# Optimization experiments

Measured on AMD Instinct MI355X. Metric: run time of the kernel, lower is better.

## Reference

```python
import jax, jax.numpy as jnp
import numpy as np

B, N, H, E = 64, 512, 32, 4
N_STEPS = 5
ANNO = 1


def setup_inputs() -> dict:
    key = jax.random.key(0)
    ks = jax.random.split(key, 20)
    sc_h = 1.0 / np.sqrt(H)
    sc_3h = 1.0 / np.sqrt(3 * H)
    sc_ha = 1.0 / np.sqrt(H + ANNO)
    inp = {
        "x": jax.random.normal(ks[0], (B, N, H), jnp.float32),
        "a": jax.random.uniform(ks[1], (B, N, ANNO), jnp.float32),
        "m": jax.random.uniform(ks[2], (B, N, 2 * N * E), jnp.float32),
        # fc_in / fc_out: hidden -> hidden*n_edge (torch Linear: W [out,in])
        "W_in": jax.random.normal(ks[3], (H * E, H), jnp.float32) * sc_h,
        "b_in": jax.random.normal(ks[4], (H * E,), jnp.float32) * sc_h,
        "W_out": jax.random.normal(ks[5], (H * E, H), jnp.float32) * sc_h,
        "b_out": jax.random.normal(ks[6], (H * E,), jnp.float32) * sc_h,
        # GRU-style gates: 3*hidden -> hidden
        "Wz": jax.random.normal(ks[7], (H, 3 * H), jnp.float32) * sc_3h,
        "bz": jax.random.normal(ks[8], (H,), jnp.float32) * sc_3h,
        "Wr": jax.random.normal(ks[9], (H, 3 * H), jnp.float32) * sc_3h,
        "br": jax.random.normal(ks[10], (H,), jnp.float32) * sc_3h,
        "Wt": jax.random.normal(ks[11], (H, 3 * H), jnp.float32) * sc_3h,
        "bt": jax.random.normal(ks[12], (H,), jnp.float32) * sc_3h,
        # output head (task_id not in {18,19}): fc1, fc2
        "W1": jax.random.normal(ks[13], (H, H + ANNO), jnp.float32) * sc_ha,
        "b1": jax.random.normal(ks[14], (H,), jnp.float32) * sc_ha,
        "W2": jax.random.normal(ks[15], (1, H), jnp.float32) * sc_h,
        "b2": jax.random.normal(ks[16], (1,), jnp.float32) * sc_h,
    }
    return inp


def _reorder(s):
    # [B, N, H*E] -> view(B,N,H,E) -> transpose(2,3) -> transpose(1,2) -> [B, E*N, H]
    return s.reshape(B, N, H, E).transpose(0, 3, 1, 2).reshape(B, E * N, H)


def reference(x, a, m, W_in, b_in, W_out, b_out, Wz, bz, Wr, br, Wt, bt, W1, b1, W2, b2):
    m_in = m[:, :, : N * E]   # [B, N, N*E]
    m_out = m[:, :, N * E :]  # [B, N, N*E]
    h = x
    for _ in range(N_STEPS):
        s_in = _reorder(h @ W_in.T + b_in)    # [B, E*N, H]
        s_out = _reorder(h @ W_out.T + b_out)  # [B, E*N, H]
        a_in = jnp.einsum("bnm,bmh->bnh", m_in, s_in)
        a_out = jnp.einsum("bnm,bmh->bnh", m_out, s_out)
        cat = jnp.concatenate([a_in, a_out, h], axis=-1)  # [B, N, 3H]
        z = jax.nn.sigmoid(cat @ Wz.T + bz)
        r = jax.nn.sigmoid(cat @ Wr.T + br)
        joint = jnp.concatenate([a_in, a_out, r * h], axis=-1)
        h_hat = jnp.tanh(joint @ Wt.T + bt)
        h = (1.0 - z) * h + z * h_hat
    out = jnp.tanh(jnp.concatenate([h, a], axis=-1) @ W1.T + b1)  # [B, N, H]
    out = (out @ W2.T + b2).sum(-1)  # [B, N]
    return out
```

## Files before the change

### kernel.cpp

```cpp
#include <hip/hip_runtime.h>
#include <hip/hip_fp16.h>
#include <math.h>

#define B_ 64
#define N_ 512
#define H_ 32
#define E_ 4
#define NSTEPS 5
#define KTOT 2048

typedef _Float16 half8 __attribute__((ext_vector_type(8)));
typedef float   f32x4 __attribute__((ext_vector_type(4)));

__global__ __launch_bounds__(256) void k_init_h(const float* __restrict__ x,
                                                float* __restrict__ h) {
    int i = blockIdx.x * blockDim.x + threadIdx.x;
    ((f32x4*)h)[i] = ((const f32x4*)x)[i];
}

__global__ __launch_bounds__(256) void k_s(const float* __restrict__ hstate,
                                           const float* __restrict__ W_in,
                                           const float* __restrict__ b_in,
                                           const float* __restrict__ W_out,
                                           const float* __restrict__ b_out,
                                           _Float16* __restrict__ sT_in_hi,
                                           _Float16* __restrict__ sT_in_lo,
                                           _Float16* __restrict__ sT_out_hi,
                                           _Float16* __restrict__ sT_out_lo) {
    int b  = blockIdx.x >> 3;
    int n0 = (blockIdx.x & 7) * 64;
    int lane = threadIdx.x & 63;
    int w = __builtin_amdgcn_readfirstlane((int)(threadIdx.x >> 6));
    int n = n0 + lane;

    const float* hrow = hstate + ((size_t)b * N_ + n) * H_;
    f32x4 hv[8];
#pragma unroll
    for (int c = 0; c < 8; c++) hv[c] = ((const f32x4*)hrow)[c];

#pragma unroll 4
    for (int o = 0; o < 32; o++) {
        int he = w * 32 + o;
        const f32x4* wr = (const f32x4*)(W_in + (size_t)he * H_);
        float acc = b_in[he];
#pragma unroll
        for (int c = 0; c < 8; c++) {
            f32x4 wv = wr[c];
            acc += hv[c][0]*wv[0] + hv[c][1]*wv[1] + hv[c][2]*wv[2] + hv[c][3]*wv[3];
        }
        int hh = he >> 2, e = he & 3;
        size_t idx = ((size_t)b * H_ + hh) * KTOT + e * N_ + n;
        _Float16 hi = (_Float16)acc;
        _Float16 lo = (_Float16)(acc - (float)hi);
        sT_in_hi[idx] = hi;
        sT_in_lo[idx] = lo;
    }
#pragma unroll 4
    for (int o = 0; o < 32; o++) {
        int he = w * 32 + o;
        const f32x4* wr = (const f32x4*)(W_out + (size_t)he * H_);
        float acc = b_out[he];
#pragma unroll
        for (int c = 0; c < 8; c++) {
            f32x4 wv = wr[c];
            acc += hv[c][0]*wv[0] + hv[c][1]*wv[1] + hv[c][2]*wv[2] + hv[c][3]*wv[3];
        }
        int hh = he >> 2, e = he & 3;
        size_t idx = ((size_t)b * H_ + hh) * KTOT + e * N_ + n;
        _Float16 hi = (_Float16)acc;
        _Float16 lo = (_Float16)(acc - (float)hi);
        sT_out_hi[idx] = hi;
        sT_out_lo[idx] = lo;
    }
}

__global__ __launch_bounds__(256) void k_einsum(const float* __restrict__ m,
                                                const _Float16* __restrict__ sT_in_hi,
                                                const _Float16* __restrict__ sT_in_lo,
                                                const _Float16* __restrict__ sT_out_hi,
                                                const _Float16* __restrict__ sT_out_lo,
                                                float* __restrict__ a_in,
                                                float* __restrict__ a_out) {
    int dir = blockIdx.z;
    int b   = blockIdx.y;
    int n0  = blockIdx.x * 64;
    int tid  = threadIdx.x;
    int w    = tid >> 6;
    int lane = tid & 63;
    int l15  = lane & 15;
    int quad = lane >> 4;

    const _Float16* sHi = (dir ? sT_out_hi : sT_in_hi) + (size_t)b * H_ * KTOT;
    const _Float16* sLo = (dir ? sT_out_lo : sT_in_lo) + (size_t)b * H_ * KTOT;
    float* aout = dir ? a_out : a_in;

    int row = n0 + w * 16 + l15;
    const float* mrow = m + ((size_t)b * N_ + row) * (2 * KTOT) + (size_t)dir * KTOT;

    f32x4 acc0 = {0.f,0.f,0.f,0.f}, acc1 = {0.f,0.f,0.f,0.f};

#pragma unroll 2
    for (int ks = 0; ks < KTOT; ks += 32) {
        int ko = ks + quad * 8;
        f32x4 a0 = *(const f32x4*)(mrow + ko);
        f32x4 a1 = *(const f32x4*)(mrow + ko + 4);
        half8 Bhi0 = *(const half8*)(sHi + (size_t)l15        * KTOT + ko);
        half8 Bhi1 = *(const half8*)(sHi + (size_t)(l15 + 16) * KTOT + ko);
        half8 Blo0 = *(const half8*)(sLo + (size_t)l15        * KTOT + ko);
        half8 Blo1 = *(const half8*)(sLo + (size_t)(l15 + 16) * KTOT + ko);

        half8 Ahi, Alo;
#pragma unroll
        for (int j = 0; j < 4; j++) {
            float v0 = a0[j], v1 = a1[j];
            _Float16 h0 = (_Float16)v0, h1 = (_Float16)v1;
            Ahi[j]     = h0;
            Ahi[j + 4] = h1;
            Alo[j]     = (_Float16)(v0 - (float)h0);
            Alo[j + 4] = (_Float16)(v1 - (float)h1);
        }
        acc0 = __builtin_amdgcn_mfma_f32_16x16x32_f16(Ahi, Bhi0, acc0, 0, 0, 0);
        acc1 = __builtin_amdgcn_mfma_f32_16x16x32_f16(Ahi, Bhi1, acc1, 0, 0, 0);
        acc0 = __builtin_amdgcn_mfma_f32_16x16x32_f16(Ahi, Blo0, acc0, 0, 0, 0);
        acc1 = __builtin_amdgcn_mfma_f32_16x16x32_f16(Ahi, Blo1, acc1, 0, 0, 0);
        acc0 = __builtin_amdgcn_mfma_f32_16x16x32_f16(Alo, Bhi0, acc0, 0, 0, 0);
        acc1 = __builtin_amdgcn_mfma_f32_16x16x32_f16(Alo, Bhi1, acc1, 0, 0, 0);
    }

#pragma unroll
    for (int r = 0; r < 4; r++) {
        size_t rr = (size_t)b * N_ + (n0 + w * 16 + quad * 4 + r);
        aout[rr * H_ + l15]      = acc0[r];
        aout[rr * H_ + 16 + l15] = acc1[r];
    }
}

__global__ __launch_bounds__(256) void k_gate(const float* __restrict__ a_in,
                                              const float* __restrict__ a_out,
                                              float* __restrict__ hstate,
                                              const float* __restrict__ Wz,
                                              const float* __restrict__ bz,
                                              const float* __restrict__ Wr,
                                              const float* __restrict__ br,
                                              const float* __restrict__ Wt,
                                              const float* __restrict__ bt) {
    __shared__ float cat[8][96];
    __shared__ float rh[8][32];
    int base = blockIdx.x * 8;
    int t = threadIdx.x;

    for (int idx = t; idx < 768; idx += 256) {
        int r = idx / 96, c = idx - r * 96;
        size_t row = (size_t)(base + r);
        float v;
        if (c < 32)      v = a_in [row * 32 + c];
        else if (c < 64) v = a_out[row * 32 + (c - 32)];
        else             v = hstate[row * 32 + (c - 64)];
        cat[r][c] = v;
    }
    __syncthreads();

    int r = t >> 5, i = t & 31;
    float az = bz[i], ar = br[i];
    const f32x4* wzr = (const f32x4*)(Wz + (size_t)i * 96);
    const f32x4* wrr = (const f32x4*)(Wr + (size_t)i * 96);
    const f32x4* crow = (const f32x4*)cat[r];
#pragma unroll
    for (int kc = 0; kc < 24; kc++) {
        f32x4 cv = crow[kc];
        f32x4 wz = wzr[kc];
        f32x4 wr = wrr[kc];
        az += cv[0]*wz[0] + cv[1]*wz[1] + cv[2]*wz[2] + cv[3]*wz[3];
        ar += cv[0]*wr[0] + cv[1]*wr[1] + cv[2]*wr[2] + cv[3]*wr[3];
    }
    float z  = 1.f / (1.f + __expf(-az));
    float rg = 1.f / (1.f + __expf(-ar));
    float hold = cat[r][64 + i];
    rh[r][i] = rg * hold;
    __syncthreads();

    float at = bt[i];
    const f32x4* wtr = (const f32x4*)(Wt + (size_t)i * 96);
#pragma unroll
    for (int kc = 0; kc < 16; kc++) {
        f32x4 cv = crow[kc];
        f32x4 wt = wtr[kc];
        at += cv[0]*wt[0] + cv[1]*wt[1] + cv[2]*wt[2] + cv[3]*wt[3];
    }
    const f32x4* rrow = (const f32x4*)rh[r];
#pragma unroll
    for (int kc = 0; kc < 8; kc++) {
        f32x4 cv = rrow[kc];
        f32x4 wt = wtr[16 + kc];
        at += cv[0]*wt[0] + cv[1]*wt[1] + cv[2]*wt[2] + cv[3]*wt[3];
    }
    float hh = tanhf(at);
    hstate[(size_t)(base + r) * 32 + i] = (1.f - z) * hold + z * hh;
}

__global__ __launch_bounds__(256) void k_final(const float* __restrict__ hstate,
                                               const float* __restrict__ a,
                                               const float* __restrict__ W1,
                                               const float* __restrict__ b1,
                                               const float* __restrict__ W2,
                                               const float* __restrict__ b2,
                                               float* __restrict__ out) {
    __shared__ float hl[8][32];
    __shared__ float as[8];
    int base = blockIdx.x * 8;
    int t = threadIdx.x;
    {
        int r = t >> 5, c = t & 31;
        hl[r][c] = hstate[(size_t)(base + r) * 32 + c];
        if (t < 8) as[t] = a[base + t];
    }
    __syncthreads();
    int r = t >> 5, j = t & 31;
    float acc = b1[j];
    const float* w1r = W1 + (size_t)j * 33;
#pragma unroll
    for (int i2 = 0; i2 < 32; i2++) acc += hl[r][i2] * w1r[i2];
    acc += as[r] * w1r[32];
    float o = tanhf(acc) * W2[j];
#pragma unroll
    for (int off = 16; off; off >>= 1) o += __shfl_xor(o, off, 32);
    if (j == 0) out[base + r] = o + b2[0];
}

extern "C" void kernel_launch(void* const* d_in, const int* in_sizes, int n_in,
                              void* d_out, int out_size, void* d_ws, size_t ws_size,
                              hipStream_t stream) {
    const float* x     = (const float*)d_in[0];
    const float* a     = (const float*)d_in[1];
    const float* m     = (const float*)d_in[2];
    const float* W_in  = (const float*)d_in[3];
    const float* b_in  = (const float*)d_in[4];
    const float* W_out = (const float*)d_in[5];
    const float* b_out = (const float*)d_in[6];
    const float* Wz    = (const float*)d_in[7];
    const float* bz    = (const float*)d_in[8];
    const float* Wr    = (const float*)d_in[9];
    const float* br    = (const float*)d_in[10];
    const float* Wt    = (const float*)d_in[11];
    const float* bt    = (const float*)d_in[12];
    const float* W1    = (const float*)d_in[13];
    const float* b1    = (const float*)d_in[14];
    const float* W2    = (const float*)d_in[15];
    const float* b2    = (const float*)d_in[16];
    float* out = (float*)d_out;

    char* ws = (char*)d_ws;
    float*    h         = (float*)(ws);
    float*    a_in      = (float*)(ws + ((size_t)4  << 20));
    float*    a_out     = (float*)(ws + ((size_t)8  << 20));
    _Float16* sT_in_hi  = (_Float16*)(ws + ((size_t)12 << 20));
    _Float16* sT_in_lo  = (_Float16*)(ws + ((size_t)20 << 20));
    _Float16* sT_out_hi = (_Float16*)(ws + ((size_t)28 << 20));
    _Float16* sT_out_lo = (_Float16*)(ws + ((size_t)36 << 20));

    k_init_h<<<1024, 256, 0, stream>>>(x, h);
    for (int s = 0; s < NSTEPS; s++) {
        k_s<<<512, 256, 0, stream>>>(h, W_in, b_in, W_out, b_out,
                                     sT_in_hi, sT_in_lo, sT_out_hi, sT_out_lo);
        k_einsum<<<dim3(8, 64, 2), 256, 0, stream>>>(m, sT_in_hi, sT_in_lo,
                                                     sT_out_hi, sT_out_lo,
                                                     a_in, a_out);
        k_gate<<<4096, 256, 0, stream>>>(a_in, a_out, h, Wz, bz, Wr, br, Wt, bt);
    }
    k_final<<<4096, 256, 0, stream>>>(h, a, W1, b1, W2, b2, out);
}
```

Baseline: 2.459 ms.

## Stage einsum tiles through LDS with direct global-to-LDS loads and double buffering

Rewrites the einsum kernel to stream m and the hi/lo fp16 s-tiles into shared memory with global_load_lds, using two buffers so the next K chunk loads while MFMAs run on the current one. An XOR swizzle on LDS addresses is meant to avoid bank conflicts on the fragment reads. The goal is to hide global memory latency and coalesce loads that previously went straight from global into registers with strided access, at the cost of about 96KB of LDS per block, which limits occupancy, plus a barrier per chunk.

```diff
diff --git a/kernel.cpp b/kernel.cpp
--- a/kernel.cpp
+++ b/kernel.cpp
@@ -11,6 +11,12 @@
 
 typedef _Float16 half8 __attribute__((ext_vector_type(8)));
 typedef float   f32x4 __attribute__((ext_vector_type(4)));
+
+__device__ __forceinline__ void gld16(const void* g, void* l) {
+    __builtin_amdgcn_global_load_lds(
+        (const __attribute__((address_space(1))) void*)g,
+        (__attribute__((address_space(3))) void*)l, 16, 0, 0);
+}
 
 __global__ __launch_bounds__(256) void k_init_h(const float* __restrict__ x,
                                                 float* __restrict__ h) {
@@ -51,9 +57,8 @@
         int hh = he >> 2, e = he & 3;
         size_t idx = ((size_t)b * H_ + hh) * KTOT + e * N_ + n;
         _Float16 hi = (_Float16)acc;
-        _Float16 lo = (_Float16)(acc - (float)hi);
         sT_in_hi[idx] = hi;
-        sT_in_lo[idx] = lo;
+        sT_in_lo[idx] = (_Float16)(acc - (float)hi);
     }
 #pragma unroll 4
     for (int o = 0; o < 32; o++) {
@@ -68,63 +73,108 @@
         int hh = he >> 2, e = he & 3;
         size_t idx = ((size_t)b * H_ + hh) * KTOT + e * N_ + n;
         _Float16 hi = (_Float16)acc;
-        _Float16 lo = (_Float16)(acc - (float)hi);
         sT_out_hi[idx] = hi;
-        sT_out_lo[idx] = lo;
-    }
-}
-
-__global__ __launch_bounds__(256) void k_einsum(const float* __restrict__ m,
-                                                const _Float16* __restrict__ sT_in_hi,
-                                                const _Float16* __restrict__ sT_in_lo,
-                                                const _Float16* __restrict__ sT_out_hi,
-                                                const _Float16* __restrict__ sT_out_lo,
-                                                float* __restrict__ a_in,
-                                                float* __restrict__ a_out) {
-    int dir = blockIdx.z;
-    int b   = blockIdx.y;
-    int n0  = blockIdx.x * 64;
+        sT_out_lo[idx] = (_Float16)(acc - (float)hi);
+    }
+}
+
+#define BUFA 32768
+#define BUFB 16384
+__global__ __launch_bounds__(256) void k_einsum_gl(const float* __restrict__ m,
+                                                   const _Float16* __restrict__ sT_in_hi,
+                                                   const _Float16* __restrict__ sT_in_lo,
+                                                   const _Float16* __restrict__ sT_out_hi,
+                                                   const _Float16* __restrict__ sT_out_lo,
+                                                   float* __restrict__ a_in,
+                                                   float* __restrict__ a_out) {
+    __shared__ __align__(16) char lds[2 * BUFA + 2 * BUFB];
+    int nblk = blockIdx.x;
+    int b    = blockIdx.y;
+    int dir  = blockIdx.z;
+    int n0   = nblk * 64;
     int tid  = threadIdx.x;
     int w    = tid >> 6;
     int lane = tid & 63;
     int l15  = lane & 15;
     int quad = lane >> 4;
 
+    const char* mBase = (const char*)(m + ((size_t)(b * N_ + n0)) * (2 * KTOT)
+                                        + (size_t)dir * KTOT);
     const _Float16* sHi = (dir ? sT_out_hi : sT_in_hi) + (size_t)b * H_ * KTOT;
     const _Float16* sLo = (dir ? sT_out_lo : sT_in_lo) + (size_t)b * H_ * KTOT;
     float* aout = dir ? a_out : a_in;
 
-    int row = n0 + w * 16 + l15;
-    const float* mrow = m + ((size_t)b * N_ + row) * (2 * KTOT) + (size_t)dir * KTOT;
+    int bp  = w >> 1;
+    int brb = (w & 1) << 4;
+    const _Float16* sP = bp ? sLo : sHi;
+
+    auto STAGE = [&](int c, int buf) {
+        char* dA = lds + buf * BUFA;
+        char* dB = lds + 2 * BUFA + buf * BUFB + bp * 8192;
+#pragma unroll
+        for (int i = 0; i < 8; i++) {
+            int r = (w << 4) + 2 * i + (lane >> 5);
+            const char* g = mBase + (size_t)r * (2 * KTOT * 4) + c * 512
+                            + (((lane & 31) * 16) ^ ((r & 7) << 4));
+            gld16(g, dA + ((w << 4) + 2 * i) * 512);
+        }
+#pragma unroll
+        for (int i = 0; i < 4; i++) {
+            int r = brb + 4 * i + (lane >> 4);
+            const char* g = (const char*)(sP + (size_t)r * KTOT) + c * 256
+                            + (((lane & 15) * 16) ^ ((r & 7) << 4));
+            gld16(g, dB + (brb + 4 * i) * 256);
+        }
+    };
 
     f32x4 acc0 = {0.f,0.f,0.f,0.f}, acc1 = {0.f,0.f,0.f,0.f};
 
-#pragma unroll 2
-    for (int ks = 0; ks < KTOT; ks += 32) {
-        int ko = ks + quad * 8;
-        f32x4 a0 = *(const f32x4*)(mrow + ko);
-        f32x4 a1 = *(const f32x4*)(mrow + ko + 4);
-        half8 Bhi0 = *(const half8*)(sHi + (size_t)l15        * KTOT + ko);
-        half8 Bhi1 = *(const half8*)(sHi + (size_t)(l15 + 16) * KTOT + ko);
-        half8 Blo0 = *(const half8*)(sLo + (size_t)l15        * KTOT + ko);
-        half8 Blo1 = *(const half8*)(sLo + (size_t)(l15 + 16) * KTOT + ko);
-
-        half8 Ahi, Alo;
-#pragma unroll
-        for (int j = 0; j < 4; j++) {
-            float v0 = a0[j], v1 = a1[j];
-            _Float16 h0 = (_Float16)v0, h1 = (_Float16)v1;
-            Ahi[j]     = h0;
-            Ahi[j + 4] = h1;
-            Alo[j]     = (_Float16)(v0 - (float)h0);
-            Alo[j + 4] = (_Float16)(v1 - (float)h1);
-        }
-        acc0 = __builtin_amdgcn_mfma_f32_16x16x32_f16(Ahi, Bhi0, acc0, 0, 0, 0);
-        acc1 = __builtin_amdgcn_mfma_f32_16x16x32_f16(Ahi, Bhi1, acc1, 0, 0, 0);
-        acc0 = __builtin_amdgcn_mfma_f32_16x16x32_f16(Ahi, Blo0, acc0, 0, 0, 0);
-        acc1 = __builtin_amdgcn_mfma_f32_16x16x32_f16(Ahi, Blo1, acc1, 0, 0, 0);
-        acc0 = __builtin_amdgcn_mfma_f32_16x16x32_f16(Alo, Bhi0, acc0, 0, 0, 0);
-        acc1 = __builtin_amdgcn_mfma_f32_16x16x32_f16(Alo, Bhi1, acc1, 0, 0, 0);
+    int rowA  = (w << 4) + l15;
+    int swzA  = (rowA & 7) << 4;
+    int swzB0 = (l15 & 7) << 4;
+
+    STAGE(0, 0);
+    __syncthreads();
+
+    for (int c = 0; c < 16; c++) {
+        int buf = c & 1;
+        if (c < 15) STAGE(c + 1, buf ^ 1);
+
+        const char* Ab = lds + buf * BUFA + rowA * 512;
+        const char* Bh = lds + 2 * BUFA + buf * BUFB;
+        const char* Bl = Bh + 8192;
+#pragma unroll
+        for (int it = 0; it < 4; it++) {
+            int kab = it * 128 + quad * 32;
+            f32x4 a0 = *(const f32x4*)(Ab + (kab ^ swzA));
+            f32x4 a1 = *(const f32x4*)(Ab + ((kab + 16) ^ swzA));
+
+            int kbb = it * 64 + quad * 16;
+            int o0 = l15 * 256        + (kbb ^ swzB0);
+            int o1 = (l15 + 16) * 256 + (kbb ^ swzB0);
+            half8 Bhi0 = *(const half8*)(Bh + o0);
+            half8 Bhi1 = *(const half8*)(Bh + o1);
+            half8 Blo0 = *(const half8*)(Bl + o0);
+            half8 Blo1 = *(const half8*)(Bl + o1);
+
+            half8 Ahi, Alo;
+#pragma unroll
+            for (int j = 0; j < 4; j++) {
+                float v0 = a0[j], v1 = a1[j];
+                _Float16 h0 = (_Float16)v0, h1 = (_Float16)v1;
+                Ahi[j]     = h0;
+                Ahi[j + 4] = h1;
+                Alo[j]     = (_Float16)(v0 - (float)h0);
+                Alo[j + 4] = (_Float16)(v1 - (float)h1);
+            }
+            acc0 = __builtin_amdgcn_mfma_f32_16x16x32_f16(Ahi, Bhi0, acc0, 0, 0, 0);
+            acc1 = __builtin_amdgcn_mfma_f32_16x16x32_f16(Ahi, Bhi1, acc1, 0, 0, 0);
+            acc0 = __builtin_amdgcn_mfma_f32_16x16x32_f16(Ahi, Blo0, acc0, 0, 0, 0);
+            acc1 = __builtin_amdgcn_mfma_f32_16x16x32_f16(Ahi, Blo1, acc1, 0, 0, 0);
+            acc0 = __builtin_amdgcn_mfma_f32_16x16x32_f16(Alo, Bhi0, acc0, 0, 0, 0);
+            acc1 = __builtin_amdgcn_mfma_f32_16x16x32_f16(Alo, Bhi1, acc1, 0, 0, 0);
+        }
+        __syncthreads();
     }
 
 #pragma unroll
@@ -262,9 +312,9 @@
     for (int s = 0; s < NSTEPS; s++) {
         k_s<<<512, 256, 0, stream>>>(h, W_in, b_in, W_out, b_out,
                                      sT_in_hi, sT_in_lo, sT_out_hi, sT_out_lo);
-        k_einsum<<<dim3(8, 64, 2), 256, 0, stream>>>(m, sT_in_hi, sT_in_lo,
-                                                     sT_out_hi, sT_out_lo,
-                                                     a_in, a_out);
+        k_einsum_gl<<<dim3(8, 64, 2), 256, 0, stream>>>(m, sT_in_hi, sT_in_lo,
+                                                        sT_out_hi, sT_out_lo,
+                                                        a_in, a_out);
         k_gate<<<4096, 256, 0, stream>>>(a_in, a_out, h, Wz, bz, Wr, br, Wt, bt);
     }
     k_final<<<4096, 256, 0, stream>>>(h, a, W1, b1, W2, b2, out);
```

Measured after the change: 2.183 ms. -11.2%, faster.
